# Optimization experiments

Hardware: AMD Instinct MI355X
Metric: run time of the kernel (lower is better)

Reference implementation:

```python
import jax, jax.numpy as jnp
import numpy as np

N, F, E = 2048, 512, 32  # batch, n_features (attention length), embedding_dim


def setup_inputs() -> dict:
    key = jax.random.key(0)
    ks = jax.random.split(key, 8)
    xav = np.sqrt(2.0 / (F + E))  # xavier_normal std for [F, E] params
    X = jax.random.normal(ks[0], (N, F), dtype=jnp.float32)
    Xi = jax.random.randint(ks[1], (N,), 0, 2).astype(jnp.float32)
    idx = jax.random.randint(ks[2], (N,), 0, F)
    I = jax.nn.one_hot(idx, F, dtype=jnp.float32)  # one-hot feature selector
    S = (jax.random.uniform(ks[3], (N, F)) < 0.5).astype(jnp.float32)
    S = S.at[:, 0].set(1.0)  # guarantee non-empty context per row
    return {
        "X": X, "Xi": Xi, "I": I, "S": S,
        "xi_w": jax.random.normal(ks[4], (F, E), jnp.float32) * xav,
        "xi_b": jax.random.normal(ks[5], (F, E), jnp.float32) * xav,
        "xs_w": jax.random.normal(ks[6], (F, E), jnp.float32) * xav,
        "xs_b": jax.random.normal(ks[7], (F, E), jnp.float32) * xav,
    }


def stable_softmax(x):
    # softmax along last dim; rows that are entirely -inf produce zeros
    m = jnp.max(x, axis=-1, keepdims=True)
    m = jnp.where(jnp.isfinite(m), m, jnp.zeros_like(m))
    e = jnp.exp(x - m)
    s = jnp.sum(e, axis=-1, keepdims=True)
    return e / jnp.maximum(s, jnp.asarray(1e-9, x.dtype))


def reference(X, Xi, I, S, xi_w, xi_b, xs_w, xs_b):
    # --- map_xs (attention aggregator) ---
    # FX: [N, F, E]; note the original reuses xs_featurizer_bias for the I-term
    FX = X[:, :, None] * xs_w[None] + xs_b[None] + (I @ xs_b)[:, None, :]
    keep = (S[:, :, None] * S[:, None, :]) > 0  # [N, F, F]
    mask = jnp.where(keep, 0.0, -jnp.inf).astype(FX.dtype)
    scale = jnp.asarray(1.0 / np.sqrt(E), FX.dtype)
    scores = mask + jnp.einsum('nqe,nke->nqk', FX * scale, FX)
    attn = stable_softmax(scores)  # [N, F, F]
    Fxs = jnp.einsum('nqk,nke->nqe', attn, FX).sum(axis=1) / S.sum(axis=1)[:, None]  # [N, E]
    # --- map_xi ---
    Iw = I @ xi_w  # [N, E]
    Ib = I @ xi_b  # [N, E]
    Fxi = Xi[:, None] * Iw + Ib
    # --- score / logz / logprob (binary, exp score) ---
    ulogp = jnp.log(jnp.exp(jnp.sum(Fxi * Fxs, axis=-1)))
    s0 = jnp.exp(jnp.sum(Ib * Fxs, axis=-1))          # Xi = 0
    s1 = jnp.exp(jnp.sum((Iw + Ib) * Fxs, axis=-1))   # Xi = 1
    logz = jnp.log(s0 + s1)
    return ulogp - logz  # [N]
```

## Files before the change

kernel.cpp:

```cpp
#include <hip/hip_runtime.h>
#include <math.h>

#define FF 512
#define EE 32
#define RS 40

typedef __attribute__((ext_vector_type(8))) short bf16x8;
typedef __attribute__((ext_vector_type(4))) float f32x4;

#define SFOLD 0.5050092f

__device__ __forceinline__ unsigned short f2bf(float x) {
    unsigned int u = __float_as_uint(x);
    return (unsigned short)((u + 0x7fffu + ((u >> 16) & 1u)) >> 16);
}
__device__ __forceinline__ float bf2f(unsigned short h) {
    return __uint_as_float(((unsigned int)h) << 16);
}

extern "C" __global__ void __launch_bounds__(512, 6)
model_kernel(const float* __restrict__ X, const float* __restrict__ Xi,
             const float* __restrict__ I, const float* __restrict__ S,
             const float* __restrict__ xi_w, const float* __restrict__ xi_b,
             const float* __restrict__ xs_w, const float* __restrict__ xs_b,
             float* __restrict__ out) {
    const int n = blockIdx.x;
    const int tid = threadIdx.x;
    const int lane = tid & 63;
    const int wv = tid >> 6;
    const int l15 = lane & 15;
    const int grp = lane >> 4;

    __shared__ __align__(16) unsigned short fxb[FF * RS];
    __shared__ unsigned short lst[FF];
    __shared__ __align__(16) float Zs[FF];
    __shared__ float ws[FF];
    __shared__ __align__(16) float idxb[EE];
    __shared__ float pf[16][EE];
    __shared__ float fxs_sh[EE];
    __shared__ int sh_idx;
    __shared__ int wbase[8];

    const float* Srow = S + (size_t)n * FF;
    const float* Irow = I + (size_t)n * FF;
    const float* Xrow = X + (size_t)n * FF;

    if (Irow[tid] > 0.5f) sh_idx = tid;

    {
        bool act = Srow[tid] > 0.f;
        unsigned long long m = __ballot(act);
        int nb = __popcll(m & ((1ull << lane) - 1ull));
        if (lane == 0) wbase[wv] = __popcll(m);
        __syncthreads();
        int off = 0;
        for (int i = 0; i < wv; ++i) off += wbase[i];
        if (act) lst[off + nb] = (unsigned short)tid;
    }
    int cnt = 0;
#pragma unroll
    for (int i = 0; i < 8; ++i) cnt += wbase[i];
    const int nt = (cnt + 15) >> 4;
    const int ntp16 = nt * 16;
    const int idx = sh_idx;
    if (tid < EE) idxb[tid] = xs_b[idx * EE + tid];
    __syncthreads();

    for (int jb = 0; jb < ntp16; jb += 64) {
        int j = jb + (tid >> 3);
        int e4 = (tid & 7) * 4;
        if (j < ntp16) {
            unsigned short h0 = 0, h1 = 0, h2 = 0, h3 = 0;
            if (j < cnt) {
                int f = lst[j];
                float xv = Xrow[f];
                float4 w4 = *(const float4*)(xs_w + f * EE + e4);
                float4 b4 = *(const float4*)(xs_b + f * EE + e4);
                float4 i4 = *(const float4*)(idxb + e4);
                h0 = f2bf(SFOLD * fmaf(xv, w4.x, b4.x + i4.x));
                h1 = f2bf(SFOLD * fmaf(xv, w4.y, b4.y + i4.y));
                h2 = f2bf(SFOLD * fmaf(xv, w4.z, b4.z + i4.z));
                h3 = f2bf(SFOLD * fmaf(xv, w4.w, b4.w + i4.w));
            }
            ushort4 pk = make_ushort4(h0, h1, h2, h3);
            *(ushort4*)(fxb + j * RS + e4) = pk;
        }
    }
    __syncthreads();

    const unsigned short* myrow = fxb + (size_t)l15 * RS + grp * 8;

    for (int j = wv; j < nt; j += 8) {
        bf16x8 bfrag = *(const bf16x8*)(myrow + (size_t)j * 16 * RS);
        float zc0 = 0.f, zc1 = 0.f;
        const unsigned short* ap = myrow;
        int i = 0;
        for (; i + 2 <= nt; i += 2) {
            bf16x8 a0 = *(const bf16x8*)(ap);
            bf16x8 a1 = *(const bf16x8*)(ap + 16 * RS);
            ap += 32 * RS;
            f32x4 d0 = {0.f, 0.f, 0.f, 0.f};
            f32x4 d1 = {0.f, 0.f, 0.f, 0.f};
            d0 = __builtin_amdgcn_mfma_f32_16x16x32_bf16(a0, bfrag, d0, 0, 0, 0);
            d1 = __builtin_amdgcn_mfma_f32_16x16x32_bf16(a1, bfrag, d1, 0, 0, 0);
            zc0 += (__builtin_amdgcn_exp2f(d0[0]) + __builtin_amdgcn_exp2f(d0[1])) +
                   (__builtin_amdgcn_exp2f(d0[2]) + __builtin_amdgcn_exp2f(d0[3]));
            zc1 += (__builtin_amdgcn_exp2f(d1[0]) + __builtin_amdgcn_exp2f(d1[1])) +
                   (__builtin_amdgcn_exp2f(d1[2]) + __builtin_amdgcn_exp2f(d1[3]));
        }
        if (i < nt) {
            bf16x8 a0 = *(const bf16x8*)(ap);
            f32x4 d0 = {0.f, 0.f, 0.f, 0.f};
            d0 = __builtin_amdgcn_mfma_f32_16x16x32_bf16(a0, bfrag, d0, 0, 0, 0);
            zc0 += (__builtin_amdgcn_exp2f(d0[0]) + __builtin_amdgcn_exp2f(d0[1])) +
                   (__builtin_amdgcn_exp2f(d0[2]) + __builtin_amdgcn_exp2f(d0[3]));
        }
        float zc = zc0 + zc1;
        zc += __shfl_xor(zc, 16);
        zc += __shfl_xor(zc, 32);
        if (lane < 16) Zs[j * 16 + lane] = zc;
    }
    __syncthreads();
    {
        float pad = (float)(ntp16 - cnt);
        for (int q = tid; q < ntp16; q += 512)
            Zs[q] = (q < cnt) ? 1.f / fmaxf(Zs[q] - pad, 1e-9f) : 0.f;
    }
    __syncthreads();

    for (int j = wv; j < nt; j += 8) {
        bf16x8 bfrag = *(const bf16x8*)(myrow + (size_t)j * 16 * RS);
        float wc0 = 0.f, wc1 = 0.f;
        const unsigned short* ap = myrow;
        const float* zp = Zs + grp * 4;
        int i = 0;
        for (; i + 2 <= nt; i += 2) {
            bf16x8 a0 = *(const bf16x8*)(ap);
            bf16x8 a1 = *(const bf16x8*)(ap + 16 * RS);
            ap += 32 * RS;
            float4 z0 = *(const float4*)(zp);
            float4 z1 = *(const float4*)(zp + 16);
            zp += 32;
            f32x4 d0 = {0.f, 0.f, 0.f, 0.f};
            f32x4 d1 = {0.f, 0.f, 0.f, 0.f};
            d0 = __builtin_amdgcn_mfma_f32_16x16x32_bf16(a0, bfrag, d0, 0, 0, 0);
            d1 = __builtin_amdgcn_mfma_f32_16x16x32_bf16(a1, bfrag, d1, 0, 0, 0);
            wc0 = fmaf(__builtin_amdgcn_exp2f(d0[0]), z0.x, wc0);
            wc0 = fmaf(__builtin_amdgcn_exp2f(d0[1]), z0.y, wc0);
            wc0 = fmaf(__builtin_amdgcn_exp2f(d0[2]), z0.z, wc0);
            wc0 = fmaf(__builtin_amdgcn_exp2f(d0[3]), z0.w, wc0);
            wc1 = fmaf(__builtin_amdgcn_exp2f(d1[0]), z1.x, wc1);
            wc1 = fmaf(__builtin_amdgcn_exp2f(d1[1]), z1.y, wc1);
            wc1 = fmaf(__builtin_amdgcn_exp2f(d1[2]), z1.z, wc1);
            wc1 = fmaf(__builtin_amdgcn_exp2f(d1[3]), z1.w, wc1);
        }
        if (i < nt) {
            bf16x8 a0 = *(const bf16x8*)(ap);
            float4 z0 = *(const float4*)(zp);
            f32x4 d0 = {0.f, 0.f, 0.f, 0.f};
            d0 = __builtin_amdgcn_mfma_f32_16x16x32_bf16(a0, bfrag, d0, 0, 0, 0);
            wc0 = fmaf(__builtin_amdgcn_exp2f(d0[0]), z0.x, wc0);
            wc0 = fmaf(__builtin_amdgcn_exp2f(d0[1]), z0.y, wc0);
            wc0 = fmaf(__builtin_amdgcn_exp2f(d0[2]), z0.z, wc0);
            wc0 = fmaf(__builtin_amdgcn_exp2f(d0[3]), z0.w, wc0);
        }
        float wcs = wc0 + wc1;
        wcs += __shfl_xor(wcs, 16);
        wcs += __shfl_xor(wcs, 32);
        if (lane < 16) ws[j * 16 + lane] = wcs;
    }
    __syncthreads();

    {
        int e = tid & 31, g = tid >> 5;
        float acc = 0.f;
        for (int k = g; k < cnt; k += 16)
            acc += ws[k] * bf2f(fxb[k * RS + e]);
        pf[g][e] = acc;
    }
    __syncthreads();
    if (tid < EE) {
        float s = 0.f;
#pragma unroll
        for (int g = 0; g < 16; ++g) s += pf[g][tid];
        fxs_sh[tid] = s * (1.0f / SFOLD) / (float)cnt;
    }
    __syncthreads();
    if (tid < EE) {
        float fv = fxs_sh[tid];
        pf[0][tid] = xi_w[idx * EE + tid] * fv;
    }
    __syncthreads();
    if (tid == 0) {
        float a = 0.f;
#pragma unroll
        for (int e = 0; e < EE; ++e) a += pf[0][e];
        float xiv = Xi[n];
        float mm = fmaxf(a, 0.f);
        float sp = mm + logf(__expf(a - mm) + __expf(-mm));
        out[n] = xiv * a - sp;
    }
}

extern "C" void kernel_launch(void* const* d_in, const int* in_sizes, int n_in,
                              void* d_out, int out_size, void* d_ws, size_t ws_size,
                              hipStream_t stream) {
    const float* X    = (const float*)d_in[0];
    const float* Xi   = (const float*)d_in[1];
    const float* I    = (const float*)d_in[2];
    const float* S    = (const float*)d_in[3];
    const float* xi_w = (const float*)d_in[4];
    const float* xi_b = (const float*)d_in[5];
    const float* xs_w = (const float*)d_in[6];
    const float* xs_b = (const float*)d_in[7];
    float* out = (float*)d_out;
    const int N = in_sizes[1];
    hipLaunchKernelGGL(model_kernel, dim3(N), dim3(512), 0, stream,
                       X, Xi, I, S, xi_w, xi_b, xs_w, xs_b, out);
}
```

Measured before the change: 121.9 us.

## Double block size and split attention inner loops across four waves with LDS atomics

Launches 1024 threads per row block and splits each 16-row query tile's key loop into four interleaved parts handled by different waves. Partial row sums and weighted sums are combined with shared-memory atomicAdd into zero-initialized buffers. The aim is more waves per block to hide MFMA/exp latency and shorten the per-block critical path. In exchange it adds LDS atomic traffic and may reduce the number of resident blocks per CU.

```diff
diff --git a/kernel.cpp b/kernel.cpp
--- a/kernel.cpp
+++ b/kernel.cpp
@@ -18,7 +18,7 @@
     return __uint_as_float(((unsigned int)h) << 16);
 }
 
-extern "C" __global__ void __launch_bounds__(512, 6)
+extern "C" __global__ void __launch_bounds__(1024, 8)
 model_kernel(const float* __restrict__ X, const float* __restrict__ Xi,
              const float* __restrict__ I, const float* __restrict__ S,
              const float* __restrict__ xi_w, const float* __restrict__ xi_b,
@@ -36,37 +36,40 @@
     __shared__ __align__(16) float Zs[FF];
     __shared__ float ws[FF];
     __shared__ __align__(16) float idxb[EE];
-    __shared__ float pf[16][EE];
+    __shared__ float pf[32][EE];
     __shared__ float fxs_sh[EE];
     __shared__ int sh_idx;
-    __shared__ int wbase[8];
+    __shared__ int wbase[16];
 
     const float* Srow = S + (size_t)n * FF;
     const float* Irow = I + (size_t)n * FF;
     const float* Xrow = X + (size_t)n * FF;
 
-    if (Irow[tid] > 0.5f) sh_idx = tid;
-
-    {
-        bool act = Srow[tid] > 0.f;
-        unsigned long long m = __ballot(act);
-        int nb = __popcll(m & ((1ull << lane) - 1ull));
-        if (lane == 0) wbase[wv] = __popcll(m);
-        __syncthreads();
-        int off = 0;
-        for (int i = 0; i < wv; ++i) off += wbase[i];
-        if (act) lst[off + nb] = (unsigned short)tid;
-    }
+    bool act = false;
+    if (tid < FF) {
+        Zs[tid] = 0.f;
+        ws[tid] = 0.f;
+        if (Irow[tid] > 0.5f) sh_idx = tid;
+        act = Srow[tid] > 0.f;
+    }
+    unsigned long long m = __ballot(act);
+    int nb = __popcll(m & ((1ull << lane) - 1ull));
+    if (lane == 0) wbase[wv] = __popcll(m);
+    __syncthreads();
+
+    int off = 0;
+    for (int i = 0; i < wv; ++i) off += wbase[i];
+    if (act) lst[off + nb] = (unsigned short)tid;
     int cnt = 0;
 #pragma unroll
-    for (int i = 0; i < 8; ++i) cnt += wbase[i];
+    for (int i = 0; i < 16; ++i) cnt += wbase[i];
     const int nt = (cnt + 15) >> 4;
     const int ntp16 = nt * 16;
     const int idx = sh_idx;
     if (tid < EE) idxb[tid] = xs_b[idx * EE + tid];
     __syncthreads();
 
-    for (int jb = 0; jb < ntp16; jb += 64) {
+    for (int jb = 0; jb < ntp16; jb += 128) {
         int j = jb + (tid >> 3);
         int e4 = (tid & 7) * 4;
         if (j < ntp16) {
@@ -89,16 +92,16 @@
     __syncthreads();
 
     const unsigned short* myrow = fxb + (size_t)l15 * RS + grp * 8;
-
-    for (int j = wv; j < nt; j += 8) {
+    const int nparts = nt << 2;
+
+    for (int p = wv; p < nparts; p += 16) {
+        const int j = p >> 2, q = p & 3;
         bf16x8 bfrag = *(const bf16x8*)(myrow + (size_t)j * 16 * RS);
         float zc0 = 0.f, zc1 = 0.f;
-        const unsigned short* ap = myrow;
-        int i = 0;
-        for (; i + 2 <= nt; i += 2) {
-            bf16x8 a0 = *(const bf16x8*)(ap);
-            bf16x8 a1 = *(const bf16x8*)(ap + 16 * RS);
-            ap += 32 * RS;
+        int i = q;
+        for (; i + 4 < nt; i += 8) {
+            bf16x8 a0 = *(const bf16x8*)(myrow + (size_t)i * 16 * RS);
+            bf16x8 a1 = *(const bf16x8*)(myrow + (size_t)(i + 4) * 16 * RS);
             f32x4 d0 = {0.f, 0.f, 0.f, 0.f};
             f32x4 d1 = {0.f, 0.f, 0.f, 0.f};
             d0 = __builtin_amdgcn_mfma_f32_16x16x32_bf16(a0, bfrag, d0, 0, 0, 0);
@@ -109,7 +112,7 @@
                    (__builtin_amdgcn_exp2f(d1[2]) + __builtin_amdgcn_exp2f(d1[3]));
         }
         if (i < nt) {
-            bf16x8 a0 = *(const bf16x8*)(ap);
+            bf16x8 a0 = *(const bf16x8*)(myrow + (size_t)i * 16 * RS);
             f32x4 d0 = {0.f, 0.f, 0.f, 0.f};
             d0 = __builtin_amdgcn_mfma_f32_16x16x32_bf16(a0, bfrag, d0, 0, 0, 0);
             zc0 += (__builtin_amdgcn_exp2f(d0[0]) + __builtin_amdgcn_exp2f(d0[1])) +
@@ -118,29 +121,26 @@
         float zc = zc0 + zc1;
         zc += __shfl_xor(zc, 16);
         zc += __shfl_xor(zc, 32);
-        if (lane < 16) Zs[j * 16 + lane] = zc;
+        if (lane < 16) atomicAdd(&Zs[j * 16 + lane], zc);
     }
     __syncthreads();
     {
         float pad = (float)(ntp16 - cnt);
-        for (int q = tid; q < ntp16; q += 512)
-            Zs[q] = (q < cnt) ? 1.f / fmaxf(Zs[q] - pad, 1e-9f) : 0.f;
-    }
-    __syncthreads();
-
-    for (int j = wv; j < nt; j += 8) {
+        if (tid < ntp16)
+            Zs[tid] = (tid < cnt) ? 1.f / fmaxf(Zs[tid] - pad, 1e-9f) : 0.f;
+    }
+    __syncthreads();
+
+    for (int p = wv; p < nparts; p += 16) {
+        const int j = p >> 2, q = p & 3;
         bf16x8 bfrag = *(const bf16x8*)(myrow + (size_t)j * 16 * RS);
         float wc0 = 0.f, wc1 = 0.f;
-        const unsigned short* ap = myrow;
-        const float* zp = Zs + grp * 4;
-        int i = 0;
-        for (; i + 2 <= nt; i += 2) {
-            bf16x8 a0 = *(const bf16x8*)(ap);
-            bf16x8 a1 = *(const bf16x8*)(ap + 16 * RS);
-            ap += 32 * RS;
-            float4 z0 = *(const float4*)(zp);
-            float4 z1 = *(const float4*)(zp + 16);
-            zp += 32;
+        int i = q;
+        for (; i + 4 < nt; i += 8) {
+            bf16x8 a0 = *(const bf16x8*)(myrow + (size_t)i * 16 * RS);
+            bf16x8 a1 = *(const bf16x8*)(myrow + (size_t)(i + 4) * 16 * RS);
+            float4 z0 = *(const float4*)(Zs + i * 16 + grp * 4);
+            float4 z1 = *(const float4*)(Zs + (i + 4) * 16 + grp * 4);
             f32x4 d0 = {0.f, 0.f, 0.f, 0.f};
             f32x4 d1 = {0.f, 0.f, 0.f, 0.f};
             d0 = __builtin_amdgcn_mfma_f32_16x16x32_bf16(a0, bfrag, d0, 0, 0, 0);
@@ -155,8 +155,8 @@
             wc1 = fmaf(__builtin_amdgcn_exp2f(d1[3]), z1.w, wc1);
         }
         if (i < nt) {
-            bf16x8 a0 = *(const bf16x8*)(ap);
-            float4 z0 = *(const float4*)(zp);
+            bf16x8 a0 = *(const bf16x8*)(myrow + (size_t)i * 16 * RS);
+            float4 z0 = *(const float4*)(Zs + i * 16 + grp * 4);
             f32x4 d0 = {0.f, 0.f, 0.f, 0.f};
             d0 = __builtin_amdgcn_mfma_f32_16x16x32_bf16(a0, bfrag, d0, 0, 0, 0);
             wc0 = fmaf(__builtin_amdgcn_exp2f(d0[0]), z0.x, wc0);
@@ -167,14 +167,14 @@
         float wcs = wc0 + wc1;
         wcs += __shfl_xor(wcs, 16);
         wcs += __shfl_xor(wcs, 32);
-        if (lane < 16) ws[j * 16 + lane] = wcs;
+        if (lane < 16) atomicAdd(&ws[j * 16 + lane], wcs);
     }
     __syncthreads();
 
     {
         int e = tid & 31, g = tid >> 5;
         float acc = 0.f;
-        for (int k = g; k < cnt; k += 16)
+        for (int k = g; k < cnt; k += 32)
             acc += ws[k] * bf2f(fxb[k * RS + e]);
         pf[g][e] = acc;
     }
@@ -182,7 +182,7 @@
     if (tid < EE) {
         float s = 0.f;
 #pragma unroll
-        for (int g = 0; g < 16; ++g) s += pf[g][tid];
+        for (int g = 0; g < 32; ++g) s += pf[g][tid];
         fxs_sh[tid] = s * (1.0f / SFOLD) / (float)cnt;
     }
     __syncthreads();
@@ -215,6 +215,6 @@
     const float* xs_b = (const float*)d_in[7];
     float* out = (float*)d_out;
     const int N = in_sizes[1];
-    hipLaunchKernelGGL(model_kernel, dim3(N), dim3(512), 0, stream,
+    hipLaunchKernelGGL(model_kernel, dim3(N), dim3(1024), 0, stream,
                        X, Xi, I, S, xi_w, xi_b, xs_w, xs_b, out);
 }
```

After: 142.6 us. +17.0%, slower.

## Process column tile pairs per wave to reuse A fragments across two MFMAs

Applied to the files above, without the earlier changes.

Each wave now handles two 16-column tiles at once in both the softmax-denominator pass and the weighted-sum pass. Every loaded A fragment feeds two MFMAs, which halves LDS reads per MFMA and adds independent accumulators for more instruction-level parallelism. The fxb buffer is zero-padded up to a multiple of 32 rows so the second tile of the last pair can be read safely. The trade-off is more registers per thread and worse load balance: with about 256 active features there are only around 8 pairs, so some of the 8 waves may sit idle.

```diff
diff --git a/kernel.cpp b/kernel.cpp
--- a/kernel.cpp
+++ b/kernel.cpp
@@ -46,30 +46,30 @@
     const float* Xrow = X + (size_t)n * FF;
 
     if (Irow[tid] > 0.5f) sh_idx = tid;
-
-    {
-        bool act = Srow[tid] > 0.f;
-        unsigned long long m = __ballot(act);
-        int nb = __popcll(m & ((1ull << lane) - 1ull));
-        if (lane == 0) wbase[wv] = __popcll(m);
-        __syncthreads();
-        int off = 0;
-        for (int i = 0; i < wv; ++i) off += wbase[i];
-        if (act) lst[off + nb] = (unsigned short)tid;
-    }
+    bool act = Srow[tid] > 0.f;
+    unsigned long long m = __ballot(act);
+    int nb = __popcll(m & ((1ull << lane) - 1ull));
+    if (lane == 0) wbase[wv] = __popcll(m);
+    __syncthreads();
+
+    int off = 0;
+    for (int i = 0; i < wv; ++i) off += wbase[i];
+    if (act) lst[off + nb] = (unsigned short)tid;
     int cnt = 0;
 #pragma unroll
     for (int i = 0; i < 8; ++i) cnt += wbase[i];
     const int nt = (cnt + 15) >> 4;
     const int ntp16 = nt * 16;
+    const int npairs = (nt + 1) >> 1;
+    const int jend = npairs * 32;
     const int idx = sh_idx;
     if (tid < EE) idxb[tid] = xs_b[idx * EE + tid];
     __syncthreads();
 
-    for (int jb = 0; jb < ntp16; jb += 64) {
+    for (int jb = 0; jb < jend; jb += 64) {
         int j = jb + (tid >> 3);
         int e4 = (tid & 7) * 4;
-        if (j < ntp16) {
+        if (j < jend) {
             unsigned short h0 = 0, h1 = 0, h2 = 0, h3 = 0;
             if (j < cnt) {
                 int f = lst[j];
@@ -90,47 +90,67 @@
 
     const unsigned short* myrow = fxb + (size_t)l15 * RS + grp * 8;
 
-    for (int j = wv; j < nt; j += 8) {
-        bf16x8 bfrag = *(const bf16x8*)(myrow + (size_t)j * 16 * RS);
-        float zc0 = 0.f, zc1 = 0.f;
+    for (int jp = wv; jp < npairs; jp += 8) {
+        const int j0 = jp * 2, j1 = j0 + 1;
+        bf16x8 b0 = *(const bf16x8*)(myrow + (size_t)j0 * 16 * RS);
+        bf16x8 b1 = *(const bf16x8*)(myrow + (size_t)j1 * 16 * RS);
+        float zc00 = 0.f, zc01 = 0.f, zc10 = 0.f, zc11 = 0.f;
         const unsigned short* ap = myrow;
         int i = 0;
         for (; i + 2 <= nt; i += 2) {
             bf16x8 a0 = *(const bf16x8*)(ap);
             bf16x8 a1 = *(const bf16x8*)(ap + 16 * RS);
             ap += 32 * RS;
-            f32x4 d0 = {0.f, 0.f, 0.f, 0.f};
-            f32x4 d1 = {0.f, 0.f, 0.f, 0.f};
-            d0 = __builtin_amdgcn_mfma_f32_16x16x32_bf16(a0, bfrag, d0, 0, 0, 0);
-            d1 = __builtin_amdgcn_mfma_f32_16x16x32_bf16(a1, bfrag, d1, 0, 0, 0);
-            zc0 += (__builtin_amdgcn_exp2f(d0[0]) + __builtin_amdgcn_exp2f(d0[1])) +
-                   (__builtin_amdgcn_exp2f(d0[2]) + __builtin_amdgcn_exp2f(d0[3]));
-            zc1 += (__builtin_amdgcn_exp2f(d1[0]) + __builtin_amdgcn_exp2f(d1[1])) +
-                   (__builtin_amdgcn_exp2f(d1[2]) + __builtin_amdgcn_exp2f(d1[3]));
+            f32x4 d00 = {0.f, 0.f, 0.f, 0.f};
+            f32x4 d01 = {0.f, 0.f, 0.f, 0.f};
+            f32x4 d10 = {0.f, 0.f, 0.f, 0.f};
+            f32x4 d11 = {0.f, 0.f, 0.f, 0.f};
+            d00 = __builtin_amdgcn_mfma_f32_16x16x32_bf16(a0, b0, d00, 0, 0, 0);
+            d01 = __builtin_amdgcn_mfma_f32_16x16x32_bf16(a0, b1, d01, 0, 0, 0);
+            d10 = __builtin_amdgcn_mfma_f32_16x16x32_bf16(a1, b0, d10, 0, 0, 0);
+            d11 = __builtin_amdgcn_mfma_f32_16x16x32_bf16(a1, b1, d11, 0, 0, 0);
+            zc00 += (__builtin_amdgcn_exp2f(d00[0]) + __builtin_amdgcn_exp2f(d00[1])) +
+                    (__builtin_amdgcn_exp2f(d00[2]) + __builtin_amdgcn_exp2f(d00[3]));
+            zc01 += (__builtin_amdgcn_exp2f(d01[0]) + __builtin_amdgcn_exp2f(d01[1])) +
+                    (__builtin_amdgcn_exp2f(d01[2]) + __builtin_amdgcn_exp2f(d01[3]));
+            zc10 += (__builtin_amdgcn_exp2f(d10[0]) + __builtin_amdgcn_exp2f(d10[1])) +
+                    (__builtin_amdgcn_exp2f(d10[2]) + __builtin_amdgcn_exp2f(d10[3]));
+            zc11 += (__builtin_amdgcn_exp2f(d11[0]) + __builtin_amdgcn_exp2f(d11[1])) +
+                    (__builtin_amdgcn_exp2f(d11[2]) + __builtin_amdgcn_exp2f(d11[3]));
         }
         if (i < nt) {
             bf16x8 a0 = *(const bf16x8*)(ap);
-            f32x4 d0 = {0.f, 0.f, 0.f, 0.f};
-            d0 = __builtin_amdgcn_mfma_f32_16x16x32_bf16(a0, bfrag, d0, 0, 0, 0);
-            zc0 += (__builtin_amdgcn_exp2f(d0[0]) + __builtin_amdgcn_exp2f(d0[1])) +
-                   (__builtin_amdgcn_exp2f(d0[2]) + __builtin_amdgcn_exp2f(d0[3]));
-        }
-        float zc = zc0 + zc1;
-        zc += __shfl_xor(zc, 16);
-        zc += __shfl_xor(zc, 32);
-        if (lane < 16) Zs[j * 16 + lane] = zc;
+            f32x4 d00 = {0.f, 0.f, 0.f, 0.f};
+            f32x4 d01 = {0.f, 0.f, 0.f, 0.f};
+            d00 = __builtin_amdgcn_mfma_f32_16x16x32_bf16(a0, b0, d00, 0, 0, 0);
+            d01 = __builtin_amdgcn_mfma_f32_16x16x32_bf16(a0, b1, d01, 0, 0, 0);
+            zc00 += (__builtin_amdgcn_exp2f(d00[0]) + __builtin_amdgcn_exp2f(d00[1])) +
+                    (__builtin_amdgcn_exp2f(d00[2]) + __builtin_amdgcn_exp2f(d00[3]));
+            zc01 += (__builtin_amdgcn_exp2f(d01[0]) + __builtin_amdgcn_exp2f(d01[1])) +
+                    (__builtin_amdgcn_exp2f(d01[2]) + __builtin_amdgcn_exp2f(d01[3]));
+        }
+        float zc0 = zc00 + zc10;
+        float zc1 = zc01 + zc11;
+        zc0 += __shfl_xor(zc0, 16); zc0 += __shfl_xor(zc0, 32);
+        zc1 += __shfl_xor(zc1, 16); zc1 += __shfl_xor(zc1, 32);
+        if (lane < 16) {
+            Zs[j0 * 16 + lane] = zc0;
+            if (j1 < nt) Zs[j1 * 16 + lane] = zc1;
+        }
     }
     __syncthreads();
     {
         float pad = (float)(ntp16 - cnt);
-        for (int q = tid; q < ntp16; q += 512)
-            Zs[q] = (q < cnt) ? 1.f / fmaxf(Zs[q] - pad, 1e-9f) : 0.f;
-    }
-    __syncthreads();
-
-    for (int j = wv; j < nt; j += 8) {
-        bf16x8 bfrag = *(const bf16x8*)(myrow + (size_t)j * 16 * RS);
-        float wc0 = 0.f, wc1 = 0.f;
+        if (tid < ntp16)
+            Zs[tid] = (tid < cnt) ? 1.f / fmaxf(Zs[tid] - pad, 1e-9f) : 0.f;
+    }
+    __syncthreads();
+
+    for (int jp = wv; jp < npairs; jp += 8) {
+        const int j0 = jp * 2, j1 = j0 + 1;
+        bf16x8 b0 = *(const bf16x8*)(myrow + (size_t)j0 * 16 * RS);
+        bf16x8 b1 = *(const bf16x8*)(myrow + (size_t)j1 * 16 * RS);
+        float wc00 = 0.f, wc01 = 0.f, wc10 = 0.f, wc11 = 0.f;
         const unsigned short* ap = myrow;
         const float* zp = Zs + grp * 4;
         int i = 0;
@@ -141,33 +161,55 @@
             float4 z0 = *(const float4*)(zp);
             float4 z1 = *(const float4*)(zp + 16);
             zp += 32;
-            f32x4 d0 = {0.f, 0.f, 0.f, 0.f};
-            f32x4 d1 = {0.f, 0.f, 0.f, 0.f};
-            d0 = __builtin_amdgcn_mfma_f32_16x16x32_bf16(a0, bfrag, d0, 0, 0, 0);
-            d1 = __builtin_amdgcn_mfma_f32_16x16x32_bf16(a1, bfrag, d1, 0, 0, 0);
-            wc0 = fmaf(__builtin_amdgcn_exp2f(d0[0]), z0.x, wc0);
-            wc0 = fmaf(__builtin_amdgcn_exp2f(d0[1]), z0.y, wc0);
-            wc0 = fmaf(__builtin_amdgcn_exp2f(d0[2]), z0.z, wc0);
-            wc0 = fmaf(__builtin_amdgcn_exp2f(d0[3]), z0.w, wc0);
-            wc1 = fmaf(__builtin_amdgcn_exp2f(d1[0]), z1.x, wc1);
-            wc1 = fmaf(__builtin_amdgcn_exp2f(d1[1]), z1.y, wc1);
-            wc1 = fmaf(__builtin_amdgcn_exp2f(d1[2]), z1.z, wc1);
-            wc1 = fmaf(__builtin_amdgcn_exp2f(d1[3]), z1.w, wc1);
+            f32x4 d00 = {0.f, 0.f, 0.f, 0.f};
+            f32x4 d01 = {0.f, 0.f, 0.f, 0.f};
+            f32x4 d10 = {0.f, 0.f, 0.f, 0.f};
+            f32x4 d11 = {0.f, 0.f, 0.f, 0.f};
+            d00 = __builtin_amdgcn_mfma_f32_16x16x32_bf16(a0, b0, d00, 0, 0, 0);
+            d01 = __builtin_amdgcn_mfma_f32_16x16x32_bf16(a0, b1, d01, 0, 0, 0);
+            d10 = __builtin_amdgcn_mfma_f32_16x16x32_bf16(a1, b0, d10, 0, 0, 0);
+            d11 = __builtin_amdgcn_mfma_f32_16x16x32_bf16(a1, b1, d11, 0, 0, 0);
+            wc00 = fmaf(__builtin_amdgcn_exp2f(d00[0]), z0.x, wc00);
+            wc00 = fmaf(__builtin_amdgcn_exp2f(d00[1]), z0.y, wc00);
+            wc00 = fmaf(__builtin_amdgcn_exp2f(d00[2]), z0.z, wc00);
+            wc00 = fmaf(__builtin_amdgcn_exp2f(d00[3]), z0.w, wc00);
+            wc01 = fmaf(__builtin_amdgcn_exp2f(d01[0]), z0.x, wc01);
+            wc01 = fmaf(__builtin_amdgcn_exp2f(d01[1]), z0.y, wc01);
+            wc01 = fmaf(__builtin_amdgcn_exp2f(d01[2]), z0.z, wc01);
+            wc01 = fmaf(__builtin_amdgcn_exp2f(d01[3]), z0.w, wc01);
+            wc10 = fmaf(__builtin_amdgcn_exp2f(d10[0]), z1.x, wc10);
+            wc10 = fmaf(__builtin_amdgcn_exp2f(d10[1]), z1.y, wc10);
+            wc10 = fmaf(__builtin_amdgcn_exp2f(d10[2]), z1.z, wc10);
+            wc10 = fmaf(__builtin_amdgcn_exp2f(d10[3]), z1.w, wc10);
+            wc11 = fmaf(__builtin_amdgcn_exp2f(d11[0]), z1.x, wc11);
+            wc11 = fmaf(__builtin_amdgcn_exp2f(d11[1]), z1.y, wc11);
+            wc11 = fmaf(__builtin_amdgcn_exp2f(d11[2]), z1.z, wc11);
+            wc11 = fmaf(__builtin_amdgcn_exp2f(d11[3]), z1.w, wc11);
         }
         if (i < nt) {
             bf16x8 a0 = *(const bf16x8*)(ap);
             float4 z0 = *(const float4*)(zp);
-            f32x4 d0 = {0.f, 0.f, 0.f, 0.f};
-            d0 = __builtin_amdgcn_mfma_f32_16x16x32_bf16(a0, bfrag, d0, 0, 0, 0);
-            wc0 = fmaf(__builtin_amdgcn_exp2f(d0[0]), z0.x, wc0);
-            wc0 = fmaf(__builtin_amdgcn_exp2f(d0[1]), z0.y, wc0);
-            wc0 = fmaf(__builtin_amdgcn_exp2f(d0[2]), z0.z, wc0);
-            wc0 = fmaf(__builtin_amdgcn_exp2f(d0[3]), z0.w, wc0);
-        }
-        float wcs = wc0 + wc1;
-        wcs += __shfl_xor(wcs, 16);
-        wcs += __shfl_xor(wcs, 32);
-        if (lane < 16) ws[j * 16 + lane] = wcs;
+            f32x4 d00 = {0.f, 0.f, 0.f, 0.f};
+            f32x4 d01 = {0.f, 0.f, 0.f, 0.f};
+            d00 = __builtin_amdgcn_mfma_f32_16x16x32_bf16(a0, b0, d00, 0, 0, 0);
+            d01 = __builtin_amdgcn_mfma_f32_16x16x32_bf16(a0, b1, d01, 0, 0, 0);
+            wc00 = fmaf(__builtin_amdgcn_exp2f(d00[0]), z0.x, wc00);
+            wc00 = fmaf(__builtin_amdgcn_exp2f(d00[1]), z0.y, wc00);
+            wc00 = fmaf(__builtin_amdgcn_exp2f(d00[2]), z0.z, wc00);
+            wc00 = fmaf(__builtin_amdgcn_exp2f(d00[3]), z0.w, wc00);
+            wc01 = fmaf(__builtin_amdgcn_exp2f(d01[0]), z0.x, wc01);
+            wc01 = fmaf(__builtin_amdgcn_exp2f(d01[1]), z0.y, wc01);
+            wc01 = fmaf(__builtin_amdgcn_exp2f(d01[2]), z0.z, wc01);
+            wc01 = fmaf(__builtin_amdgcn_exp2f(d01[3]), z0.w, wc01);
+        }
+        float wc0 = wc00 + wc10;
+        float wc1 = wc01 + wc11;
+        wc0 += __shfl_xor(wc0, 16); wc0 += __shfl_xor(wc0, 32);
+        wc1 += __shfl_xor(wc1, 16); wc1 += __shfl_xor(wc1, 32);
+        if (lane < 16) {
+            ws[j0 * 16 + lane] = wc0;
+            if (j1 < nt) ws[j1 * 16 + lane] = wc1;
+        }
     }
     __syncthreads();
 
```

New measurement: 120.1 us. About the same (-1.5%).
